# Kernel optimization log

Hardware: AMD Instinct MI355X
Metric: run time of the kernel (lower is better)

## Reference

```python
import jax, jax.numpy as jnp
import numpy as np

N = 4_000_000      # batch of scalar angles (x[i].item() loop in the torch code)
DEPTH = 10         # qsp_depth -> 2*DEPTH+1 = 21 phase params


def setup_inputs() -> dict:
    key = jax.random.key(0)
    k1, k2, k3 = jax.random.split(key, 3)
    x = jax.random.normal(k1, (N,), dtype=jnp.float32)
    qsp_params = jax.random.uniform(k2, (2 * DEPTH + 1,), dtype=jnp.float32,
                                    minval=0.0, maxval=2.0 * np.pi)
    alphas = jax.random.uniform(k3, (N,), dtype=jnp.float32, minval=0.5, maxval=1.5)
    return {"x": x, "qsp_params": qsp_params, "alphas": alphas}


def _qsp_expectation(x, qsp_params):
    """Standard QSP: U = S(phi_0) prod_{k=1..2d} [W(theta) S(phi_k)], return Re(U[0,0]).
    W(theta) = [[cos t, i sin t], [i sin t, cos t]],  S(phi) = diag(e^{i phi}, e^{-i phi}).
    Vectorized over the batch; lax.scan over the 2*depth phase steps."""
    cc = x.astype(jnp.complex64)
    c = jnp.cos(cc)
    isn = 1j * jnp.sin(cc)
    # signal operator per sample, constant across depth steps: [N, 2, 2]
    W = jnp.stack([jnp.stack([c, isn], -1), jnp.stack([isn, c], -1)], -2)
    ph = jnp.exp(1j * qsp_params.astype(jnp.complex64))  # [2d+1]
    d0 = jnp.stack([ph[0], jnp.conj(ph[0])])             # diag of S(phi_0)
    M0 = jnp.broadcast_to(jnp.eye(2, dtype=jnp.complex64) * d0, W.shape)  # [N,2,2]

    def step(M, p):
        d = jnp.stack([p, jnp.conj(p)])                  # diag of S(phi_k)
        M = jnp.einsum('nij,njk->nik', M, W) * d         # M @ W @ S(phi_k)
        return M, None

    M, _ = jax.lax.scan(step, M0, ph[1:])
    return jnp.real(M[:, 0, 0]).astype(jnp.float32)      # Re(<0|U|0>)


def reference(x, qsp_params, alphas):
    # matches torch: preds[i] = alphas[i] * expectation_value(qsp_params, x[i]); unsqueeze(1)
    return (alphas * _qsp_expectation(x, qsp_params))[:, None]
```

## Files before the change

kernel.cpp:

```cpp
#include <hip/hip_runtime.h>

#define NPARAMS 21
#define VPT 4

__global__ __launch_bounds__(256) void qsp_kernel(
    const float* __restrict__ x,
    const float* __restrict__ qsp,
    const float* __restrict__ alphas,
    float* __restrict__ out,
    int n)
{
    __shared__ float cph[NPARAMS];
    __shared__ float sph[NPARAMS];
    const int t = threadIdx.x;
    if (t < NPARAMS) {
        float p = qsp[t];
        float sv, cv;
        __sincosf(p, &sv, &cv);
        cph[t] = cv;
        sph[t] = sv;
    }
    __syncthreads();

    const int base = (blockIdx.x * blockDim.x + t) * VPT;
    if (base >= n) return;

    const float4 xv = *reinterpret_cast<const float4*>(x + base);
    const float4 av = *reinterpret_cast<const float4*>(alphas + base);

    float xs[VPT] = {xv.x, xv.y, xv.z, xv.w};
    float al[VPT] = {av.x, av.y, av.z, av.w};

    float c[VPT], s[VPT];
    float ar[VPT], ai[VPT], br[VPT], bi[VPT];

    const float c0 = cph[0];
    const float s0 = sph[0];
#pragma unroll
    for (int j = 0; j < VPT; ++j) {
        __sincosf(xs[j], &s[j], &c[j]);
        ar[j] = c0;
        ai[j] = s0;
        br[j] = 0.0f;
        bi[j] = 0.0f;
    }

#pragma unroll
    for (int k = 1; k < NPARAMS; ++k) {
        const float cp = cph[k];
        const float sp = sph[k];
#pragma unroll
        for (int j = 0; j < VPT; ++j) {
            const float t1r = c[j] * ar[j] - s[j] * bi[j];
            const float t1i = c[j] * ai[j] + s[j] * br[j];
            const float t2r = c[j] * br[j] - s[j] * ai[j];
            const float t2i = c[j] * bi[j] + s[j] * ar[j];
            ar[j] = cp * t1r - sp * t1i;
            ai[j] = cp * t1i + sp * t1r;
            br[j] = cp * t2r + sp * t2i;
            bi[j] = cp * t2i - sp * t2r;
        }
    }

    float4 o;
    o.x = al[0] * ar[0];
    o.y = al[1] * ar[1];
    o.z = al[2] * ar[2];
    o.w = al[3] * ar[3];
    *reinterpret_cast<float4*>(out + base) = o;
}

extern "C" void kernel_launch(void* const* d_in, const int* in_sizes, int n_in,
                              void* d_out, int out_size, void* d_ws, size_t ws_size,
                              hipStream_t stream)
{
    const float* x      = (const float*)d_in[0];
    const float* qsp    = (const float*)d_in[1];
    const float* alphas = (const float*)d_in[2];
    float* out          = (float*)d_out;

    const int n = in_sizes[0];
    const int threads = 256;
    const int nthreads = (n + VPT - 1) / VPT;
    const int blocks = (nthreads + threads - 1) / threads;

    qsp_kernel<<<blocks, threads, 0, stream>>>(x, qsp, alphas, out, n);
}
```

Baseline: 95.78 us.

## Replace per-sample QSP matrix product with precomputed trig polynomial evaluation

Re(U00) is a degree-10 trigonometric polynomial in x. A tiny first kernel samples it at 21 points and computes Fourier coefficients by a DFT into workspace. The main kernel then evaluates the polynomial per sample using a Chebyshev-style recurrence from one sin/cos, instead of 20 complex 2x2 products. This is exact in exact arithmetic, but it adds a second launch and may lose some float accuracy.

```diff
diff --git a/kernel.cpp b/kernel.cpp
--- a/kernel.cpp
+++ b/kernel.cpp
@@ -2,71 +2,121 @@
 
 #define NPARAMS 21
 #define VPT 4
+#define INV_2PI 0.15915494309189535f
+#define INV_PI  0.3183098861837907f
 
-__global__ __launch_bounds__(256) void qsp_kernel(
+__device__ __forceinline__ float sin_rev(float rev) {
+    return __builtin_amdgcn_sinf(__builtin_amdgcn_fractf(rev));
+}
+__device__ __forceinline__ float cos_rev(float rev) {
+    return __builtin_amdgcn_cosf(__builtin_amdgcn_fractf(rev));
+}
+
+__global__ void coeff_kernel(const float* __restrict__ qsp, float* __restrict__ ws)
+{
+    __shared__ float g[NPARAMS];
+    const int t = threadIdx.x;
+
+    if (t < NPARAMS) {
+        const float rev_x = (float)t * (1.0f / 42.0f);
+        const float c = cos_rev(rev_x);
+        const float s = sin_rev(rev_x);
+
+        float pr = qsp[0] * INV_2PI;
+        float ar = cos_rev(pr), ai = sin_rev(pr);
+        float br = 0.0f, bi = 0.0f;
+
+        for (int k = 1; k < NPARAMS; ++k) {
+            const float pk = qsp[k] * INV_2PI;
+            const float cp = cos_rev(pk);
+            const float sp = sin_rev(pk);
+            const float t1r = c * ar - s * bi;
+            const float t1i = c * ai + s * br;
+            const float t2r = c * br - s * ai;
+            const float t2i = c * bi + s * ar;
+            ar = cp * t1r - sp * t1i;
+            ai = cp * t1i + sp * t1r;
+            br = cp * t2r + sp * t2i;
+            bi = cp * t2i - sp * t2r;
+        }
+        g[t] = ar;
+    }
+    __syncthreads();
+
+    if (t < 24) {
+        float coef = 0.0f;
+        if (t == 0) {
+            float acc = 0.0f;
+            for (int i = 0; i < NPARAMS; ++i) acc += g[i];
+            coef = acc * (1.0f / 21.0f);
+        } else if (t <= 10) {
+            float acc = 0.0f;
+            for (int i = 0; i < NPARAMS; ++i)
+                acc += g[i] * cos_rev((float)(t * i) * (1.0f / 21.0f));
+            coef = acc * (2.0f / 21.0f);
+        } else if (t <= 20) {
+            const int j = t - 10;
+            float acc = 0.0f;
+            for (int i = 0; i < NPARAMS; ++i)
+                acc += g[i] * sin_rev((float)(j * i) * (1.0f / 21.0f));
+            coef = acc * (2.0f / 21.0f);
+        }
+        ws[t] = coef;
+    }
+}
+
+__global__ __launch_bounds__(256) void eval_kernel(
     const float* __restrict__ x,
-    const float* __restrict__ qsp,
     const float* __restrict__ alphas,
+    const float* __restrict__ coefs,
     float* __restrict__ out,
     int n)
 {
-    __shared__ float cph[NPARAMS];
-    __shared__ float sph[NPARAMS];
-    const int t = threadIdx.x;
-    if (t < NPARAMS) {
-        float p = qsp[t];
-        float sv, cv;
-        __sincosf(p, &sv, &cv);
-        cph[t] = cv;
-        sph[t] = sv;
+    const int base = (blockIdx.x * blockDim.x + threadIdx.x) * VPT;
+    if (base >= n) return;
+
+    float w[24];
+    {
+        const float4* c4 = reinterpret_cast<const float4*>(coefs);
+#pragma unroll
+        for (int i = 0; i < 6; ++i) {
+            const float4 v = c4[i];
+            w[4 * i + 0] = v.x; w[4 * i + 1] = v.y;
+            w[4 * i + 2] = v.z; w[4 * i + 3] = v.w;
+        }
     }
-    __syncthreads();
-
-    const int base = (blockIdx.x * blockDim.x + t) * VPT;
-    if (base >= n) return;
 
     const float4 xv = *reinterpret_cast<const float4*>(x + base);
     const float4 av = *reinterpret_cast<const float4*>(alphas + base);
+    const float xs[VPT] = {xv.x, xv.y, xv.z, xv.w};
+    const float al[VPT] = {av.x, av.y, av.z, av.w};
+    float res[VPT];
 
-    float xs[VPT] = {xv.x, xv.y, xv.z, xv.w};
-    float al[VPT] = {av.x, av.y, av.z, av.w};
-
-    float c[VPT], s[VPT];
-    float ar[VPT], ai[VPT], br[VPT], bi[VPT];
-
-    const float c0 = cph[0];
-    const float s0 = sph[0];
 #pragma unroll
     for (int j = 0; j < VPT; ++j) {
-        __sincosf(xs[j], &s[j], &c[j]);
-        ar[j] = c0;
-        ai[j] = s0;
-        br[j] = 0.0f;
-        bi[j] = 0.0f;
-    }
+        const float f  = __builtin_amdgcn_fractf(xs[j] * INV_PI);
+        const float s1 = __builtin_amdgcn_sinf(f);
+        const float c1 = __builtin_amdgcn_cosf(f);
+        const float tc = c1 + c1;
 
+        float accP = w[0] + w[1] * c1;
+        float accQ = w[11] * s1;
+        float cpp = 1.0f, cp = c1;
+        float spp = 0.0f, sp = s1;
 #pragma unroll
-    for (int k = 1; k < NPARAMS; ++k) {
-        const float cp = cph[k];
-        const float sp = sph[k];
-#pragma unroll
-        for (int j = 0; j < VPT; ++j) {
-            const float t1r = c[j] * ar[j] - s[j] * bi[j];
-            const float t1i = c[j] * ai[j] + s[j] * br[j];
-            const float t2r = c[j] * br[j] - s[j] * ai[j];
-            const float t2i = c[j] * bi[j] + s[j] * ar[j];
-            ar[j] = cp * t1r - sp * t1i;
-            ai[j] = cp * t1i + sp * t1r;
-            br[j] = cp * t2r + sp * t2i;
-            bi[j] = cp * t2i - sp * t2r;
+        for (int k = 2; k <= 10; ++k) {
+            const float cn = tc * cp - cpp;
+            const float sn = tc * sp - spp;
+            accP += w[k] * cn;
+            accQ += w[10 + k] * sn;
+            cpp = cp; cp = cn;
+            spp = sp; sp = sn;
         }
+        res[j] = al[j] * (accP + accQ);
     }
 
     float4 o;
-    o.x = al[0] * ar[0];
-    o.y = al[1] * ar[1];
-    o.z = al[2] * ar[2];
-    o.w = al[3] * ar[3];
+    o.x = res[0]; o.y = res[1]; o.z = res[2]; o.w = res[3];
     *reinterpret_cast<float4*>(out + base) = o;
 }
 
@@ -78,11 +128,14 @@
     const float* qsp    = (const float*)d_in[1];
     const float* alphas = (const float*)d_in[2];
     float* out          = (float*)d_out;
+    float* wsf          = (float*)d_ws;
 
     const int n = in_sizes[0];
-    const int threads = 256;
+
+    coeff_kernel<<<1, 64, 0, stream>>>(qsp, wsf);
+
+    const int threads  = 256;
     const int nthreads = (n + VPT - 1) / VPT;
-    const int blocks = (nthreads + threads - 1) / threads;
-
-    qsp_kernel<<<blocks, threads, 0, stream>>>(x, qsp, alphas, out, n);
+    const int blocks   = (nthreads + threads - 1) / threads;
+    eval_kernel<<<blocks, threads, 0, stream>>>(x, alphas, wsf, out, n);
 }
```

Result: faster. 84.02 us (-12.3%).
